# Performance work log

Hardware: AMD Instinct MI355X
Metric: run time of the kernel (lower is better)

The kernel has to match this reference:

```python
import jax, jax.numpy as jnp
import numpy as np

N = 100000      # nodes
E = 1600000     # edges
F_IN = 128      # num_feat
H = 128         # hidden_dim
EMB = 64        # node_embedding_dim
HL = 256        # hidden_dim_linear


def setup_inputs() -> dict:
    key = jax.random.key(0)
    ks = jax.random.split(key, 12)
    def w(k, fan_in, shape):
        return jax.random.normal(k, shape, dtype=jnp.float32) / np.sqrt(fan_in)
    x = jax.random.normal(ks[0], (N, F_IN), dtype=jnp.float32)
    edge_index = jax.random.randint(ks[1], (2, E), 0, N, dtype=jnp.int32)
    return {
        "x": x,
        "edge_index": edge_index,
        "W0": w(ks[2], F_IN, (F_IN, H)), "b0": jnp.zeros((H,), jnp.float32),
        "W1": w(ks[3], H, (H, H)),       "b1": jnp.zeros((H,), jnp.float32),
        "W2": w(ks[4], H, (H, EMB)),     "b2": jnp.zeros((EMB,), jnp.float32),
        "lw1": w(ks[5], 2 * EMB, (2 * EMB, HL)), "lb1": jnp.zeros((HL,), jnp.float32),
        "lw2": w(ks[6], HL, (HL, 1)),            "lb2": jnp.zeros((1,), jnp.float32),
    }


def _gcn_forward(x, edge_index, W0, b0, W1, b1, W2, b2, lw1, lb1, lw2, lb2):
    src, dst = edge_index[0], edge_index[1]
    # add self loops (PyG GCNConv default) -- shared across layers
    loop = jnp.arange(N, dtype=src.dtype)
    s = jnp.concatenate([src, loop])
    d = jnp.concatenate([dst, loop])
    # symmetric normalization: deg counts incoming edges incl. self loop (>=1)
    deg = jax.ops.segment_sum(jnp.ones_like(d, dtype=x.dtype), d, num_segments=N)
    norm = jax.lax.rsqrt(deg[s] * deg[d])  # [E+N]

    def conv(h, W, b):
        hw = h @ W                                   # small GEMM [N, out]
        msg = hw[s] * norm[:, None]                  # gather + scale [E+N, out]
        agg = jax.ops.segment_sum(msg, d, num_segments=N)
        return agg + b

    z = jax.nn.relu(conv(x, W0, b0))
    z = jax.nn.relu(conv(z, W1, b1))
    z = jax.nn.relu(conv(z, W2, b2))                 # [N, EMB]  (dropout: eval mode, no-op)

    # edge classifier: gather both endpoints, cat, MLP, sigmoid
    h = jnp.concatenate([z[src], z[dst]], axis=1)    # [E, 2*EMB]
    h = jax.nn.relu(h @ lw1 + lb1)
    return jax.nn.sigmoid(h @ lw2 + lb2)             # [E, 1]


def reference(x, edge_index, W0, b0, W1, b1, W2, b2, lw1, lb1, lw2, lb2):
    return _gcn_forward(x, edge_index, W0, b0, W1, b1, W2, b2, lw1, lb1, lw2, lb2)
```

## Files before the change

### kernel.cpp

```cpp
#include <hip/hip_runtime.h>

#define NNODES 100000
#define NEDGES 1600000

typedef __attribute__((ext_vector_type(8))) short bf16x8;
typedef __attribute__((ext_vector_type(4))) float f32x4;

__device__ __forceinline__ unsigned short f2bf(float f) {
  unsigned int u = __float_as_uint(f);
  u = (u + 0x7FFFu + ((u >> 16) & 1u)) >> 16;
  return (unsigned short)u;
}
__device__ __forceinline__ float bf2f(unsigned short h) {
  return __uint_as_float(((unsigned int)h) << 16);
}

__global__ void count_kernel(const int* __restrict__ dst, int* __restrict__ cntD) {
  int e = blockIdx.x * 256 + threadIdx.x;
  if (e < NEDGES) atomicAdd(&cntD[dst[e]], 1);
}

__global__ void alloc_kernel(const int* __restrict__ cntD, int* __restrict__ startD,
                             int* __restrict__ curD, float* __restrict__ dis,
                             int* __restrict__ totD) {
  int v = blockIdx.x * 256 + threadIdx.x;
  if (v < NNODES) {
    int c = cntD[v];
    int s = atomicAdd(totD, c);
    startD[v] = s;
    curD[v] = s;
    dis[v] = rsqrtf((float)(c + 1));
  }
}

__global__ void fill_kernel(const int* __restrict__ src, const int* __restrict__ dst,
                            int* __restrict__ curD, int2* __restrict__ csrPair) {
  int e = blockIdx.x * 256 + threadIdx.x;
  if (e < NEDGES) {
    int s = src[e], d = dst[e];
    int pd = atomicAdd(&curD[d], 1);
    csrPair[pd] = make_int2(s, e);
  }
}

template <int K, int HOUT>
__global__ void pack_w_kernel(const float* __restrict__ W, unsigned short* __restrict__ Wp) {
  int idx = blockIdx.x * 256 + threadIdx.x;
  if (idx < K * HOUT) {
    int k = idx / HOUT, c = idx - k * HOUT;
    Wp[((size_t)((k >> 5) * HOUT + c)) * 32 + (k & 31)] = f2bf(W[idx]);
  }
}

__global__ void pack_lw1_kernel(const float* __restrict__ lw1, const float* __restrict__ lb1,
                                unsigned short* __restrict__ Wp, float* __restrict__ biasAB) {
  int idx = blockIdx.x * 256 + threadIdx.x;
  if (idx < 64 * 512) {
    int k = idx / 512, c = idx - k * 512;
    float v = (c < 256) ? lw1[k * 256 + c] : lw1[(64 + k) * 256 + (c - 256)];
    Wp[((size_t)((k >> 5) * 512 + c)) * 32 + (k & 31)] = f2bf(v);
  }
  if (idx < 512) biasAB[idx] = (idx < 256) ? lb1[idx] : 0.0f;
}

__global__ void cvt_x_kernel(const float* __restrict__ x, unsigned short* __restrict__ hi,
                             unsigned short* __restrict__ lo) {
  int idx = blockIdx.x * 256 + threadIdx.x;
  if (idx < NNODES * 32) {
    float4 v = ((const float4*)x)[idx];
    ushort4 h, l;
    h.x = f2bf(v.x); l.x = f2bf(v.x - bf2f(h.x));
    h.y = f2bf(v.y); l.y = f2bf(v.y - bf2f(h.y));
    h.z = f2bf(v.z); l.z = f2bf(v.z - bf2f(h.z));
    h.w = f2bf(v.w); l.w = f2bf(v.w - bf2f(h.w));
    ((ushort4*)hi)[idx] = h;
    ((ushort4*)lo)[idx] = l;
  }
}

template <int K, int HOUT, bool SCALE, bool BIAS>
__global__ __launch_bounds__(256)
void mgemm_kernel(const unsigned short* __restrict__ Xhi, const unsigned short* __restrict__ Xlo,
                  const unsigned short* __restrict__ Wp, const float* __restrict__ dis,
                  const float* __restrict__ bias, unsigned short* __restrict__ outb) {
  constexpr int KC = K / 32;
  const int tid = threadIdx.x;
  const int wave = tid >> 6;
  const int lane = tid & 63;
  const int lrow = lane & 15;
  const int lsub = lane >> 4;
  const int rowBase = blockIdx.x * 64 + wave * 16;
  int arow = rowBase + lrow;
  if (arow > NNODES - 1) arow = NNODES - 1;
  bf16x8 ahi[KC], alo[KC];
#pragma unroll
  for (int kc = 0; kc < KC; ++kc) {
    ahi[kc] = *(const bf16x8*)&Xhi[(size_t)arow * K + kc * 32 + lsub * 8];
    alo[kc] = *(const bf16x8*)&Xlo[(size_t)arow * K + kc * 32 + lsub * 8];
  }
  int orow[4];
  float dis4[4];
#pragma unroll
  for (int i = 0; i < 4; ++i) {
    orow[i] = rowBase + lsub * 4 + i;
    int rc = orow[i] < NNODES ? orow[i] : NNODES - 1;
    dis4[i] = SCALE ? dis[rc] : 1.0f;
  }
  for (int ct = 0; ct < HOUT / 16; ++ct) {
    int c = ct * 16 + lrow;
    f32x4 acc = {0.f, 0.f, 0.f, 0.f};
#pragma unroll
    for (int kc = 0; kc < KC; ++kc) {
      bf16x8 b = *(const bf16x8*)&Wp[((size_t)(kc * HOUT + c)) * 32 + lsub * 8];
      acc = __builtin_amdgcn_mfma_f32_16x16x32_bf16(ahi[kc], b, acc, 0, 0, 0);
      acc = __builtin_amdgcn_mfma_f32_16x16x32_bf16(alo[kc], b, acc, 0, 0, 0);
    }
    float bb = BIAS ? bias[c] : 0.0f;
#pragma unroll
    for (int i = 0; i < 4; ++i) {
      if (orow[i] < NNODES) {
        float v = acc[i];
        if (SCALE) v *= dis4[i];
        if (BIAS) v += bb;
        outb[(size_t)orow[i] * HOUT + c] = f2bf(v);
      }
    }
  }
}

template <int HOUT>
__global__ __launch_bounds__(256)
void agg_kernel(const unsigned short* __restrict__ hws, const int2* __restrict__ csrPair,
                const int* __restrict__ startA, const int* __restrict__ cnt,
                const float* __restrict__ dis, const float* __restrict__ bias,
                unsigned short* __restrict__ outHi, unsigned short* __restrict__ outLo) {
  int gid = blockIdx.x * 256 + threadIdx.x;
  int v = gid >> 6;
  int lane = gid & 63;
  constexpr int PER = HOUT / 64;
  float acc0 = 0.0f, acc1 = 0.0f;
  if constexpr (PER == 2) {
    unsigned int o = *(const unsigned int*)&hws[(size_t)v * HOUT + lane * 2];
    acc0 = __uint_as_float(o << 16);
    acc1 = __uint_as_float(o & 0xffff0000u);
  } else {
    acc0 = bf2f(hws[(size_t)v * HOUT + lane]);
  }
  int s0 = startA[v], c = cnt[v];
  for (int base = 0; base < c; base += 64) {
    int rem = c - base;
    int m = rem < 64 ? rem : 64;
    int idx = 0;
    if (lane < m) idx = csrPair[s0 + base + lane].x;
    int j = 0;
    for (; j + 4 <= m; j += 4) {
      int u0 = __shfl(idx, j);
      int u1 = __shfl(idx, j + 1);
      int u2 = __shfl(idx, j + 2);
      int u3 = __shfl(idx, j + 3);
      if constexpr (PER == 2) {
        unsigned int r0 = *(const unsigned int*)&hws[(size_t)u0 * HOUT + lane * 2];
        unsigned int r1 = *(const unsigned int*)&hws[(size_t)u1 * HOUT + lane * 2];
        unsigned int r2 = *(const unsigned int*)&hws[(size_t)u2 * HOUT + lane * 2];
        unsigned int r3 = *(const unsigned int*)&hws[(size_t)u3 * HOUT + lane * 2];
        acc0 += __uint_as_float(r0 << 16) + __uint_as_float(r1 << 16) +
                __uint_as_float(r2 << 16) + __uint_as_float(r3 << 16);
        acc1 += __uint_as_float(r0 & 0xffff0000u) + __uint_as_float(r1 & 0xffff0000u) +
                __uint_as_float(r2 & 0xffff0000u) + __uint_as_float(r3 & 0xffff0000u);
      } else {
        float r0 = bf2f(hws[(size_t)u0 * HOUT + lane]);
        float r1 = bf2f(hws[(size_t)u1 * HOUT + lane]);
        float r2 = bf2f(hws[(size_t)u2 * HOUT + lane]);
        float r3 = bf2f(hws[(size_t)u3 * HOUT + lane]);
        acc0 += (r0 + r1) + (r2 + r3);
      }
    }
    for (; j < m; ++j) {
      int u = __shfl(idx, j);
      if constexpr (PER == 2) {
        unsigned int r = *(const unsigned int*)&hws[(size_t)u * HOUT + lane * 2];
        acc0 += __uint_as_float(r << 16);
        acc1 += __uint_as_float(r & 0xffff0000u);
      } else {
        acc0 += bf2f(hws[(size_t)u * HOUT + lane]);
      }
    }
  }
  float d = dis[v];
  if constexpr (PER == 2) {
    float o0 = fmaf(d, acc0, bias[lane * 2]);
    float o1 = fmaf(d, acc1, bias[lane * 2 + 1]);
    o0 = o0 > 0.0f ? o0 : 0.0f;
    o1 = o1 > 0.0f ? o1 : 0.0f;
    ushort2 h, l;
    h.x = f2bf(o0); l.x = f2bf(o0 - bf2f(h.x));
    h.y = f2bf(o1); l.y = f2bf(o1 - bf2f(h.y));
    *(ushort2*)&outHi[(size_t)v * HOUT + lane * 2] = h;
    *(ushort2*)&outLo[(size_t)v * HOUT + lane * 2] = l;
  } else {
    float o0 = fmaf(d, acc0, bias[lane]);
    o0 = o0 > 0.0f ? o0 : 0.0f;
    unsigned short h = f2bf(o0);
    outHi[(size_t)v * HOUT + lane] = h;
    outLo[(size_t)v * HOUT + lane] = f2bf(o0 - bf2f(h));
  }
}

__global__ __launch_bounds__(256)
void edge_kernel(const unsigned short* __restrict__ AB,
                 const int2* __restrict__ csrPair,
                 const int* __restrict__ startD, const int* __restrict__ cntD,
                 const float* __restrict__ lw2,
                 float* __restrict__ out) {
  int gid = blockIdx.x * 256 + threadIdx.x;
  int v = gid >> 6;
  int lane = gid & 63;
  int sub = lane & 15;
  const unsigned int* Brow = (const unsigned int*)&AB[(size_t)v * 512 + 256 + sub * 16];
  uint4 br0 = *(const uint4*)Brow;
  uint4 br1 = *(const uint4*)(Brow + 4);
  float bq[16];
  {
    unsigned int u[8] = {br0.x, br0.y, br0.z, br0.w, br1.x, br1.y, br1.z, br1.w};
#pragma unroll
    for (int i = 0; i < 8; ++i) {
      bq[2 * i]     = __uint_as_float(u[i] << 16);
      bq[2 * i + 1] = __uint_as_float(u[i] & 0xffff0000u);
    }
  }
  float wv[16];
#pragma unroll
  for (int i = 0; i < 4; ++i) {
    float4 w4 = *(const float4*)&lw2[sub * 16 + i * 4];
    wv[4 * i] = w4.x; wv[4 * i + 1] = w4.y; wv[4 * i + 2] = w4.z; wv[4 * i + 3] = w4.w;
  }

  int s0 = startD[v], c = cntD[v];
  for (int base = 0; base < c; base += 64) {
    int rem = c - base;
    int m = rem < 64 ? rem : 64;
    int sj = 0, ej = 0;
    if (lane < m) {
      int2 p = csrPair[s0 + base + lane];
      sj = p.x; ej = p.y;
    }
    for (int j = 0; j < m; j += 4) {
      int ls = j + (lane >> 4);
      int lsc = ls < m ? ls : m - 1;
      int s = __shfl(sj, lsc);
      int e = __shfl(ej, lsc);
      const unsigned int* Arow = (const unsigned int*)&AB[(size_t)(unsigned)s * 512 + sub * 16];
      uint4 a0 = *(const uint4*)Arow;
      uint4 a1 = *(const uint4*)(Arow + 4);
      unsigned int au[8] = {a0.x, a0.y, a0.z, a0.w, a1.x, a1.y, a1.z, a1.w};
      float p0 = 0.f, p1 = 0.f, p2 = 0.f, p3 = 0.f;
#pragma unroll
      for (int i = 0; i < 4; ++i) {
        float hlo0 = __uint_as_float(au[2 * i] << 16) + bq[4 * i];
        float hhi0 = __uint_as_float(au[2 * i] & 0xffff0000u) + bq[4 * i + 1];
        float hlo1 = __uint_as_float(au[2 * i + 1] << 16) + bq[4 * i + 2];
        float hhi1 = __uint_as_float(au[2 * i + 1] & 0xffff0000u) + bq[4 * i + 3];
        hlo0 = hlo0 > 0.f ? hlo0 : 0.f;
        hhi0 = hhi0 > 0.f ? hhi0 : 0.f;
        hlo1 = hlo1 > 0.f ? hlo1 : 0.f;
        hhi1 = hhi1 > 0.f ? hhi1 : 0.f;
        p0 = fmaf(hlo0, wv[4 * i], p0);
        p1 = fmaf(hhi0, wv[4 * i + 1], p1);
        p2 = fmaf(hlo1, wv[4 * i + 2], p2);
        p3 = fmaf(hhi1, wv[4 * i + 3], p3);
      }
      float acc = (p0 + p1) + (p2 + p3);
      acc += __shfl_xor(acc, 1);
      acc += __shfl_xor(acc, 2);
      acc += __shfl_xor(acc, 4);
      acc += __shfl_xor(acc, 8);
      if (ls < m && sub == 0) out[e] = acc;
    }
  }
}

__global__ __launch_bounds__(256)
void sigmoid_kernel(float* __restrict__ out, const float* __restrict__ lb2) {
  int i = blockIdx.x * 256 + threadIdx.x;
  if (i < NEDGES) {
    float lb = lb2[0];
    out[i] = 1.0f / (1.0f + expf(-(out[i] + lb)));
  }
}

extern "C" void kernel_launch(void* const* d_in, const int* in_sizes, int n_in,
                              void* d_out, int out_size, void* d_ws, size_t ws_size,
                              hipStream_t stream) {
  const float* x   = (const float*)d_in[0];
  const int*   ei  = (const int*)d_in[1];
  const float* W0  = (const float*)d_in[2];
  const float* b0  = (const float*)d_in[3];
  const float* W1  = (const float*)d_in[4];
  const float* b1  = (const float*)d_in[5];
  const float* W2  = (const float*)d_in[6];
  const float* b2  = (const float*)d_in[7];
  const float* lw1 = (const float*)d_in[8];
  const float* lb1 = (const float*)d_in[9];
  const float* lw2 = (const float*)d_in[10];
  const float* lb2 = (const float*)d_in[11];
  float* out = (float*)d_out;
  const int* src = ei;
  const int* dst = ei + NEDGES;

  char* ws = (char*)d_ws;
  size_t off = 0;
  auto alloc = [&](size_t bytes) -> void* {
    void* p = ws + off;
    off += (bytes + 255) & ~(size_t)255;
    return p;
  };
  int*   cntD   = (int*)alloc((size_t)NNODES * 4);
  int*   startD = (int*)alloc((size_t)NNODES * 4);
  int*   curD   = (int*)alloc((size_t)NNODES * 4);
  float* dis    = (float*)alloc((size_t)NNODES * 4);
  int*   totD   = (int*)alloc(256);
  int2*  csrPair= (int2*)alloc((size_t)NEDGES * 8);
  unsigned short* P16  = (unsigned short*)alloc((size_t)NNODES * 128 * 2);
  unsigned short* XQhi = (unsigned short*)alloc((size_t)NNODES * 128 * 2);
  unsigned short* XQlo = (unsigned short*)alloc((size_t)NNODES * 128 * 2);
  unsigned short* AB   = (unsigned short*)alloc((size_t)NNODES * 512 * 2);
  unsigned short* Wp0  = (unsigned short*)alloc((size_t)128 * 128 * 2);
  unsigned short* Wp1  = (unsigned short*)alloc((size_t)128 * 128 * 2);
  unsigned short* Wp2  = (unsigned short*)alloc((size_t)128 * 64 * 2);
  unsigned short* WpE  = (unsigned short*)alloc((size_t)64 * 512 * 2);
  float* biasAB = (float*)alloc(512 * 4);

  hipMemsetAsync(cntD, 0, (size_t)NNODES * 4, stream);
  hipMemsetAsync(totD, 0, 256, stream);
  count_kernel<<<(NEDGES + 255) / 256, 256, 0, stream>>>(dst, cntD);
  alloc_kernel<<<(NNODES + 255) / 256, 256, 0, stream>>>(cntD, startD, curD, dis, totD);
  fill_kernel<<<(NEDGES + 255) / 256, 256, 0, stream>>>(src, dst, curD, csrPair);

  pack_w_kernel<128, 128><<<64, 256, 0, stream>>>(W0, Wp0);
  pack_w_kernel<128, 128><<<64, 256, 0, stream>>>(W1, Wp1);
  pack_w_kernel<128, 64><<<32, 256, 0, stream>>>(W2, Wp2);
  pack_lw1_kernel<<<128, 256, 0, stream>>>(lw1, lb1, WpE, biasAB);
  cvt_x_kernel<<<(NNODES * 32 + 255) / 256, 256, 0, stream>>>(x, XQhi, XQlo);

  const int GB = (NNODES + 63) / 64;
  const int AB_ = (NNODES * 64) / 256;

  mgemm_kernel<128, 128, true, false><<<GB, 256, 0, stream>>>(XQhi, XQlo, Wp0, dis, nullptr, P16);
  agg_kernel<128><<<AB_, 256, 0, stream>>>(P16, csrPair, startD, cntD, dis, b0, XQhi, XQlo);
  mgemm_kernel<128, 128, true, false><<<GB, 256, 0, stream>>>(XQhi, XQlo, Wp1, dis, nullptr, P16);
  agg_kernel<128><<<AB_, 256, 0, stream>>>(P16, csrPair, startD, cntD, dis, b1, XQhi, XQlo);
  mgemm_kernel<128, 64, true, false><<<GB, 256, 0, stream>>>(XQhi, XQlo, Wp2, dis, nullptr, P16);
  agg_kernel<64><<<AB_, 256, 0, stream>>>(P16, csrPair, startD, cntD, dis, b2, XQhi, XQlo);

  mgemm_kernel<64, 512, false, true><<<GB, 256, 0, stream>>>(XQhi, XQlo, WpE, nullptr, biasAB, AB);

  edge_kernel<<<AB_, 256, 0, stream>>>(AB, csrPair, startD, cntD, lw2, out);
  sigmoid_kernel<<<(NEDGES + 255) / 256, 256, 0, stream>>>(out, lb2);
}
```

Measured before the change: 685.1 us.

## Build CSR with prefix-scan offsets and destination-sliced atomic count/fill passes

```diff
diff --git a/kernel.cpp b/kernel.cpp
--- a/kernel.cpp
+++ b/kernel.cpp
@@ -2,6 +2,9 @@
 
 #define NNODES 100000
 #define NEDGES 1600000
+#define NBLK 391
+#define NSLICE 8
+#define SLICEW 12500
 
 typedef __attribute__((ext_vector_type(8))) short bf16x8;
 typedef __attribute__((ext_vector_type(4))) float f32x4;
@@ -16,17 +19,61 @@
 }
 
 __global__ void count_kernel(const int* __restrict__ dst, int* __restrict__ cntD) {
-  int e = blockIdx.x * 256 + threadIdx.x;
-  if (e < NEDGES) atomicAdd(&cntD[dst[e]], 1);
-}
-
-__global__ void alloc_kernel(const int* __restrict__ cntD, int* __restrict__ startD,
-                             int* __restrict__ curD, float* __restrict__ dis,
-                             int* __restrict__ totD) {
+  int slice = blockIdx.x & (NSLICE - 1);
+  int e = (blockIdx.x >> 3) * 256 + threadIdx.x;
+  if (e >= NEDGES) return;
+  int d = dst[e];
+  int lo = slice * SLICEW;
+  if (d >= lo && d < lo + SLICEW) atomicAdd(&cntD[d], 1);
+}
+
+__global__ void scanA_kernel(const int* __restrict__ cntD, int* __restrict__ blockSum) {
+  __shared__ int sh[256];
   int v = blockIdx.x * 256 + threadIdx.x;
+  sh[threadIdx.x] = (v < NNODES) ? cntD[v] : 0;
+  __syncthreads();
+  for (int off = 128; off; off >>= 1) {
+    if (threadIdx.x < off) sh[threadIdx.x] += sh[threadIdx.x + off];
+    __syncthreads();
+  }
+  if (threadIdx.x == 0) blockSum[blockIdx.x] = sh[0];
+}
+
+__global__ void scanB_kernel(int* __restrict__ blockSum) {
+  int lane = threadIdx.x;
+  int carry = 0;
+  for (int base = 0; base < NBLK; base += 64) {
+    int i = base + lane;
+    int c = (i < NBLK) ? blockSum[i] : 0;
+    int pre = c;
+#pragma unroll
+    for (int off = 1; off < 64; off <<= 1) {
+      int t = __shfl_up(pre, off);
+      if (lane >= off) pre += t;
+    }
+    int tot = __shfl(pre, 63);
+    if (i < NBLK) blockSum[i] = carry + pre - c;
+    carry += tot;
+  }
+}
+
+__global__ void scanC_kernel(const int* __restrict__ cntD, const int* __restrict__ blockSum,
+                             int* __restrict__ startD, int* __restrict__ curD,
+                             float* __restrict__ dis) {
+  __shared__ int sh[256];
+  int tid = threadIdx.x;
+  int v = blockIdx.x * 256 + tid;
+  int c = (v < NNODES) ? cntD[v] : 0;
+  sh[tid] = c;
+  __syncthreads();
+  for (int off = 1; off < 256; off <<= 1) {
+    int t = (tid >= off) ? sh[tid - off] : 0;
+    __syncthreads();
+    sh[tid] += t;
+    __syncthreads();
+  }
   if (v < NNODES) {
-    int c = cntD[v];
-    int s = atomicAdd(totD, c);
+    int s = blockSum[blockIdx.x] + sh[tid] - c;
     startD[v] = s;
     curD[v] = s;
     dis[v] = rsqrtf((float)(c + 1));
@@ -35,12 +82,15 @@
 
 __global__ void fill_kernel(const int* __restrict__ src, const int* __restrict__ dst,
                             int* __restrict__ curD, int2* __restrict__ csrPair) {
-  int e = blockIdx.x * 256 + threadIdx.x;
-  if (e < NEDGES) {
-    int s = src[e], d = dst[e];
-    int pd = atomicAdd(&curD[d], 1);
-    csrPair[pd] = make_int2(s, e);
-  }
+  int slice = blockIdx.x & (NSLICE - 1);
+  int e = (blockIdx.x >> 3) * 256 + threadIdx.x;
+  if (e >= NEDGES) return;
+  int d = dst[e];
+  int lo = slice * SLICEW;
+  if (d < lo || d >= lo + SLICEW) return;
+  int s = src[e];
+  int pd = atomicAdd(&curD[d], 1);
+  csrPair[pd] = make_int2(s, e);
 }
 
 template <int K, int HOUT>
@@ -318,7 +368,7 @@
   int*   startD = (int*)alloc((size_t)NNODES * 4);
   int*   curD   = (int*)alloc((size_t)NNODES * 4);
   float* dis    = (float*)alloc((size_t)NNODES * 4);
-  int*   totD   = (int*)alloc(256);
+  int*   blockSum = (int*)alloc((size_t)NBLK * 4);
   int2*  csrPair= (int2*)alloc((size_t)NEDGES * 8);
   unsigned short* P16  = (unsigned short*)alloc((size_t)NNODES * 128 * 2);
   unsigned short* XQhi = (unsigned short*)alloc((size_t)NNODES * 128 * 2);
@@ -330,11 +380,14 @@
   unsigned short* WpE  = (unsigned short*)alloc((size_t)64 * 512 * 2);
   float* biasAB = (float*)alloc(512 * 4);
 
+  const int EB8 = NSLICE * ((NEDGES + 255) / 256);
+
   hipMemsetAsync(cntD, 0, (size_t)NNODES * 4, stream);
-  hipMemsetAsync(totD, 0, 256, stream);
-  count_kernel<<<(NEDGES + 255) / 256, 256, 0, stream>>>(dst, cntD);
-  alloc_kernel<<<(NNODES + 255) / 256, 256, 0, stream>>>(cntD, startD, curD, dis, totD);
-  fill_kernel<<<(NEDGES + 255) / 256, 256, 0, stream>>>(src, dst, curD, csrPair);
+  count_kernel<<<EB8, 256, 0, stream>>>(dst, cntD);
+  scanA_kernel<<<NBLK, 256, 0, stream>>>(cntD, blockSum);
+  scanB_kernel<<<1, 64, 0, stream>>>(blockSum);
+  scanC_kernel<<<NBLK, 256, 0, stream>>>(cntD, blockSum, startD, curD, dis);
+  fill_kernel<<<EB8, 256, 0, stream>>>(src, dst, curD, csrPair);
 
   pack_w_kernel<128, 128><<<64, 256, 0, stream>>>(W0, Wp0);
   pack_w_kernel<128, 128><<<64, 256, 0, stream>>>(W1, Wp1);
```

After: 615.7 us. -10.1%, faster.
